# Kernel tuning notes

Measured on AMD Instinct MI355X. Metric: run time of the kernel, lower is better.

## Reference

```python
import jax, jax.numpy as jnp
import numpy as np

# model / batch constants (match init_kwargs and input_specs)
H, D = 32, 128              # num_heads, head_dim
SCALE = 1.0 / float(np.sqrt(D))
BS = 16                     # paged KV-cache block size
NUM_FILL_SEQS, FILL_LEN = 4, 512
NF = NUM_FILL_SEQS * FILL_LEN          # 2048 total fill tokens
G = 16                                  # decode (Generate) sequences
BLOCKS_PER_SEQ = 64
CTX = BLOCKS_PER_SEQ * BS               # 1024 context tokens per decode seq
NB = 1280                               # total cache blocks
T = NF + G                              # 2064 total new tokens this iteration


def setup_inputs() -> dict:
    key = jax.random.key(0)
    kq, kk, kv, kkc, kvc = jax.random.split(key, 5)
    q = jax.random.normal(kq, (T, H, D), jnp.float32)
    k = jax.random.normal(kk, (T, H, D), jnp.float32)
    v = jax.random.normal(kv, (T, H, D), jnp.float32)
    k_cache = jax.random.normal(kkc, (NB, BS, H, D), jnp.float32)
    v_cache = jax.random.normal(kvc, (NB, BS, H, D), jnp.float32)
    # Fill tokens occupy contiguous slots 0..NF-1 (blocks 0..NF/BS-1)
    fill_slots = np.arange(NF, dtype=np.int64)
    # Decode seq g owns blocks [NF/BS + g*BLOCKS_PER_SEQ, ... + BLOCKS_PER_SEQ)
    first_gen_block = NF // BS
    bt = (first_gen_block
          + np.arange(G)[:, None] * BLOCKS_PER_SEQ
          + np.arange(BLOCKS_PER_SEQ)[None, :])            # [G, BLOCKS_PER_SEQ]
    # each decode's new token goes in the last slot of its context
    last = CTX - 1
    gen_slots = bt[:, last // BS] * BS + (last % BS)
    slot_mapping = jnp.asarray(
        np.concatenate([fill_slots, gen_slots]).astype(np.int32))
    block_tables = jnp.asarray(bt.astype(np.int32))
    context_lens = jnp.asarray(np.full((G,), CTX, dtype=np.int32))
    return dict(q=q, k=k, v=v, k_cache=k_cache, v_cache=v_cache,
                slot_mapping=slot_mapping, block_tables=block_tables,
                context_lens=context_lens)


def reference(q, k, v, k_cache, v_cache, slot_mapping, block_tables, context_lens):
    nb, bs = k_cache.shape[0], k_cache.shape[1]
    # vllm_reshape_and_cache: scatter new K/V into the blocked cache by slot id
    kc = k_cache.reshape(nb * bs, H, D).at[slot_mapping].set(k)
    vc = v_cache.reshape(nb * bs, H, D).at[slot_mapping].set(v)
    kcb = kc.reshape(nb, bs, H, D)
    vcb = vc.reshape(nb, bs, H, D)

    # ---- Fill: block-diagonal causal attention (q_len == kv_len fast path) ----
    qf = q[:NF].reshape(NUM_FILL_SEQS, FILL_LEN, H, D)
    kf = k[:NF].reshape(NUM_FILL_SEQS, FILL_LEN, H, D)
    vf = v[:NF].reshape(NUM_FILL_SEQS, FILL_LEN, H, D)
    s = jnp.einsum('bqhd,bkhd->bhqk', qf, kf) * SCALE
    causal = jnp.tril(jnp.ones((FILL_LEN, FILL_LEN), dtype=bool))
    s = jnp.where(causal, s, jnp.finfo(s.dtype).min)
    p = jax.nn.softmax(s, axis=-1)
    fill_out = jnp.einsum('bhqk,bkhd->bqhd', p, vf).reshape(NF, H, D)

    # ---- Generate: vLLM paged attention (1 query token per seq) ----
    qg = q[NF:]                                        # [G, H, D]
    keys = kcb[block_tables].reshape(G, -1, H, D)      # [G, CTX, H, D]
    vals = vcb[block_tables].reshape(G, -1, H, D)
    sg = jnp.einsum('ghd,gshd->ghs', qg, keys) * SCALE
    valid = jnp.arange(keys.shape[1], dtype=jnp.int32)[None, :] < context_lens[:, None]
    sg = jnp.where(valid[:, None, :], sg, jnp.finfo(sg.dtype).min)
    pg = jax.nn.softmax(sg, axis=-1)
    gen_out = jnp.einsum('ghs,gshd->ghd', pg, vals)    # [G, H, D]

    out = jnp.concatenate([fill_out, gen_out], axis=0)
    return out.reshape(T, H * D)
```

## Files before the change

### kernel.cpp

```cpp
#include <hip/hip_runtime.h>
#include <hip/hip_bf16.h>

#define HH 32
#define DD 128
#define HD (HH*DD)
#define NFILL 2048
#define FLEN 512
#define SCALE_F 0.08838834764831845f
#define NEGINF (-1e30f)
#define PSTRIDE 136

typedef short bf16x8 __attribute__((ext_vector_type(8)));
typedef float f32x4 __attribute__((ext_vector_type(4)));

__device__ __forceinline__ short f2bf(float x) {
    union { float f; unsigned u; } c; c.f = x;
    unsigned u = c.u;
    u += 0x7FFFu + ((u >> 16) & 1u);
    return (short)(u >> 16);
}

__device__ __forceinline__ bf16x8 load8_bf16(const float* __restrict__ p) {
    float4 a = *(const float4*)p;
    float4 b = *(const float4*)(p + 4);
    bf16x8 r;
    r[0]=f2bf(a.x); r[1]=f2bf(a.y); r[2]=f2bf(a.z); r[3]=f2bf(a.w);
    r[4]=f2bf(b.x); r[5]=f2bf(b.y); r[6]=f2bf(b.z); r[7]=f2bf(b.w);
    return r;
}

__global__ __launch_bounds__(256)
void gen_kernel(const float* __restrict__ q, const float* __restrict__ k,
                const float* __restrict__ v, const float* __restrict__ kc,
                const float* __restrict__ vc, const int* __restrict__ btab,
                const int* __restrict__ ctxlens, float* __restrict__ ws)
{
    __shared__ int sblk[64];
    __shared__ float accs[16][DD];
    __shared__ float marr[16], larr[16];

    const int bid  = blockIdx.x;
    const int g    = bid >> 6;
    const int h    = (bid >> 1) & 31;
    const int half = bid & 1;
    const int wv   = threadIdx.x >> 6;
    const int lane = threadIdx.x & 63;
    const int g16  = lane >> 4;
    const int li   = lane & 15;
    const int ctx  = ctxlens[g];

    if (threadIdx.x < 64) sblk[threadIdx.x] = btab[g * 64 + threadIdx.x];
    __syncthreads();

    const long qoff = (long)(NFILL + g) * HD + h * DD;
    float qr[8];
    {
        float4 a  = *(const float4*)(q + qoff + li * 8);
        float4 b2 = *(const float4*)(q + qoff + li * 8 + 4);
        qr[0]=a.x; qr[1]=a.y; qr[2]=a.z; qr[3]=a.w;
        qr[4]=b2.x; qr[5]=b2.y; qr[6]=b2.z; qr[7]=b2.w;
    }

    float m = NEGINF, l = 0.f;
    float o[8];
    #pragma unroll
    for (int j = 0; j < 8; ++j) o[j] = 0.f;

    const int wbase = half * 512 + wv * 128;

    #pragma unroll 1
    for (int c = 0; c < 8; ++c) {
        const int pb = wbase + c * 16 + g16 * 4;
        f32x4 ka[4][2], va[4][2];
        #pragma unroll
        for (int i = 0; i < 4; ++i) {
            const int p = pb + i;
            const float* kb; const float* vb;
            if (p == ctx - 1) {
                kb = k + qoff; vb = v + qoff;
            } else {
                const int slot = sblk[p >> 4] * 16 + (p & 15);
                kb = kc + (long)slot * HD + h * DD;
                vb = vc + (long)slot * HD + h * DD;
            }
            ka[i][0] = __builtin_nontemporal_load((const f32x4*)(kb + li * 8));
            ka[i][1] = __builtin_nontemporal_load((const f32x4*)(kb + li * 8 + 4));
            va[i][0] = __builtin_nontemporal_load((const f32x4*)(vb + li * 8));
            va[i][1] = __builtin_nontemporal_load((const f32x4*)(vb + li * 8 + 4));
        }
        float s[4];
        #pragma unroll
        for (int i = 0; i < 4; ++i) {
            float d0 = ka[i][0][0]*qr[0] + ka[i][0][1]*qr[1] + ka[i][0][2]*qr[2] + ka[i][0][3]*qr[3]
                     + ka[i][1][0]*qr[4] + ka[i][1][1]*qr[5] + ka[i][1][2]*qr[6] + ka[i][1][3]*qr[7];
            d0 += __shfl_xor(d0, 1);
            d0 += __shfl_xor(d0, 2);
            d0 += __shfl_xor(d0, 4);
            d0 += __shfl_xor(d0, 8);
            s[i] = d0 * SCALE_F;
        }
        const float mn = fmaxf(m, fmaxf(fmaxf(s[0], s[1]), fmaxf(s[2], s[3])));
        const float sc = __expf(m - mn);
        const float p0 = __expf(s[0] - mn);
        const float p1 = __expf(s[1] - mn);
        const float p2 = __expf(s[2] - mn);
        const float p3 = __expf(s[3] - mn);
        l = l * sc + (p0 + p1 + p2 + p3);
        #pragma unroll
        for (int j = 0; j < 4; ++j) {
            o[j] = o[j]*sc + p0*va[0][0][j] + p1*va[1][0][j]
                           + p2*va[2][0][j] + p3*va[3][0][j];
            o[j+4] = o[j+4]*sc + p0*va[0][1][j] + p1*va[1][1][j]
                               + p2*va[2][1][j] + p3*va[3][1][j];
        }
        m = mn;
    }

    const int pid = wv * 4 + g16;
    #pragma unroll
    for (int j = 0; j < 8; ++j) accs[pid][li * 8 + j] = o[j];
    if (li == 0) { marr[pid] = m; larr[pid] = l; }
    __syncthreads();

    if (threadIdx.x < DD) {
        const int d = threadIdx.x;
        float M = NEGINF;
        #pragma unroll
        for (int t = 0; t < 16; ++t) M = fmaxf(M, marr[t]);
        float L = 0.f, a = 0.f;
        #pragma unroll
        for (int t = 0; t < 16; ++t) {
            const float cc = __expf(marr[t] - M);
            L += cc * larr[t];
            a += cc * accs[t][d];
        }
        const long base = (long)(((g * 32 + h) * 2) + half) * PSTRIDE;
        ws[base + 8 + d] = a;
        if (d == 0) { ws[base] = M; ws[base + 1] = L; }
    }
}

__global__ __launch_bounds__(256)
void merge_kernel(const float* __restrict__ ws, float* __restrict__ out)
{
    const int idx = blockIdx.x * 256 + threadIdx.x;
    const int gh  = idx >> 7;
    const int d   = idx & 127;
    const int g   = gh >> 5;
    const int h   = gh & 31;
    const long b0 = (long)gh * 2 * PSTRIDE;
    const long b1 = b0 + PSTRIDE;
    const float m0 = ws[b0], l0 = ws[b0 + 1];
    const float m1 = ws[b1], l1 = ws[b1 + 1];
    const float M  = fmaxf(m0, m1);
    const float e0 = __expf(m0 - M), e1 = __expf(m1 - M);
    const float num = e0 * ws[b0 + 8 + d] + e1 * ws[b1 + 8 + d];
    const float den = e0 * l0 + e1 * l1;
    out[(long)(NFILL + g) * 4096 + h * DD + d] = num / den;
}

struct QS {
    bf16x8 qf[4];
    float  mrow[4], lsum[4];
    f32x4  o[8];
};

__device__ __forceinline__ void qs_init(QS& S, const float* qbase, int g16) {
    #pragma unroll
    for (int c = 0; c < 4; ++c) S.qf[c] = load8_bf16(qbase + c * 32 + g16 * 8);
    #pragma unroll
    for (int r = 0; r < 4; ++r) { S.mrow[r] = NEGINF; S.lsum[r] = 0.f; }
    #pragma unroll
    for (int n = 0; n < 8; ++n) { S.o[n][0]=0.f; S.o[n][1]=0.f; S.o[n][2]=0.f; S.o[n][3]=0.f; }
}

__device__ __forceinline__ void qs_tile(QS& S, int qt, int k0, int sub,
                                        const char* Kl, const char* Vt2,
                                        char* pbase, int g16, int li) {
    f32x4 sA; sA[0]=0.f; sA[1]=0.f; sA[2]=0.f; sA[3]=0.f;
    f32x4 sB; sB[0]=0.f; sB[1]=0.f; sB[2]=0.f; sB[3]=0.f;
    const int r0 = sub * 32;
    #pragma unroll
    for (int c = 0; c < 4; ++c) {
        const int rA = r0 + li, rB = r0 + li + 16;
        bf16x8 kfA = *(const bf16x8*)(Kl + ((rA * 256 + c * 64 + g16 * 16) ^ ((rA & 7) << 4)));
        bf16x8 kfB = *(const bf16x8*)(Kl + ((rB * 256 + c * 64 + g16 * 16) ^ ((rB & 7) << 4)));
        sA = __builtin_amdgcn_mfma_f32_16x16x32_bf16(S.qf[c], kfA, sA, 0, 0, 0);
        sB = __builtin_amdgcn_mfma_f32_16x16x32_bf16(S.qf[c], kfB, sB, 0, 0, 0);
    }
    float pA[4], pB[4], corr[4];
    #pragma unroll
    for (int r = 0; r < 4; ++r) {
        const int qrow = qt * 16 + g16 * 4 + r;
        float a  = (k0 + li      <= qrow) ? sA[r] * SCALE_F : NEGINF;
        float bb = (k0 + 16 + li <= qrow) ? sB[r] * SCALE_F : NEGINF;
        float rm = fmaxf(a, bb);
        #pragma unroll
        for (int off = 1; off < 16; off <<= 1) rm = fmaxf(rm, __shfl_xor(rm, off));
        const float mn = fmaxf(S.mrow[r], rm);
        corr[r] = __expf(S.mrow[r] - mn);
        pA[r] = __expf(a  - mn);
        pB[r] = __expf(bb - mn);
        float rs = pA[r] + pB[r];
        #pragma unroll
        for (int off = 1; off < 16; off <<= 1) rs += __shfl_xor(rs, off);
        S.lsum[r] = S.lsum[r] * corr[r] + rs;
        S.mrow[r] = mn;
    }
    #pragma unroll
    for (int n = 0; n < 8; ++n)
        #pragma unroll
        for (int r = 0; r < 4; ++r) S.o[n][r] *= corr[r];

    #pragma unroll
    for (int r = 0; r < 4; ++r) {
        const int row = g16 * 4 + r;
        const int xo  = (row & 3) << 4;
        *(short*)(pbase + ((row * 64 + li * 2     ) ^ xo)) = f2bf(pA[r]);
        *(short*)(pbase + ((row * 64 + 32 + li * 2) ^ xo)) = f2bf(pB[r]);
    }
    asm volatile("s_waitcnt lgkmcnt(0)" ::: "memory");
    __builtin_amdgcn_sched_barrier(0);
    bf16x8 pa = *(const bf16x8*)(pbase + ((li * 64 + g16 * 16) ^ ((li & 3) << 4)));

    const int obase = (sub * 4 + g16) * 256 + li * 16;
    #pragma unroll
    for (int n = 0; n < 8; ++n) {
        bf16x8 vf = *(const bf16x8*)(Vt2 + (n * 2048 + obase));
        S.o[n] = __builtin_amdgcn_mfma_f32_16x16x32_bf16(pa, vf, S.o[n], 0, 0, 0);
    }
}

__device__ __forceinline__ void qs_out(QS& S, int qt, int b, int h, int g16, int li,
                                       float* __restrict__ out) {
    float inv[4];
    #pragma unroll
    for (int r = 0; r < 4; ++r) inv[r] = 1.f / S.lsum[r];
    #pragma unroll
    for (int n = 0; n < 8; ++n) {
        #pragma unroll
        for (int r = 0; r < 4; ++r) {
            const int t = b * FLEN + qt * 16 + g16 * 4 + r;
            out[(long)t * 4096 + h * DD + n * 16 + li] = S.o[n][r] * inv[r];
        }
    }
}

__global__ void __launch_bounds__(512, 2)
fill_kernel(const float* __restrict__ q, const float* __restrict__ k,
            const float* __restrict__ v, float* __restrict__ out)
{
    __shared__ short Kl[64 * 128];
    __shared__ short Vt2[8 * 8 * 16 * 8];
    __shared__ short plds[8][16][32];

    const int bid = blockIdx.x;
    const int b   = bid >> 6;
    const int h   = (bid >> 1) & 31;
    const int jh  = bid & 1;
    const int tid  = threadIdx.x;
    const int wv   = tid >> 6;
    const int lane = tid & 63;
    const int g16  = lane >> 4;
    const int li   = lane & 15;

    const int qtA = 2 * wv + jh;
    const int qtB = 31 - qtA;
    const int npA = qtA / 2 + 1;
    const int npB = qtB / 2 + 1;

    QS SA, SB2;
    qs_init(SA,  q + ((long)(b * FLEN + qtA * 16 + li) * HH + h) * DD, g16);
    qs_init(SB2, q + ((long)(b * FLEN + qtB * 16 + li) * HH + h) * DD, g16);

    const int spos = tid >> 4;
    const int sd8  = tid & 15;
    const int vd   = tid & 127;
    const int voct = tid >> 7;

    char* pbase = (char*)&plds[wv][0][0];

    for (int kp = 0; kp < 8; ++kp) {
        const int k0 = kp * 64;
        #pragma unroll
        for (int rr = 0; rr < 2; ++rr) {
            const int row = spos + rr * 32;
            const float* src = k + ((long)(b * FLEN + k0 + row) * HH + h) * DD + sd8 * 8;
            bf16x8 w = load8_bf16(src);
            const int base = row * 256 + sd8 * 16;
            *(bf16x8*)((char*)Kl + (base ^ ((row & 7) << 4))) = w;
        }
        #pragma unroll
        for (int oo = 0; oo < 2; ++oo) {
            const int oct = voct + oo * 4;
            const float* src = v + ((long)(b * FLEN + k0 + oct * 8) * HH + h) * DD + vd;
            bf16x8 w;
            #pragma unroll
            for (int jj = 0; jj < 8; ++jj)
                w[jj] = f2bf(src[(long)jj * HD]);
            *(bf16x8*)((char*)Vt2 + ((vd >> 4) * 2048 + oct * 256 + (vd & 15) * 16)) = w;
        }
        __syncthreads();

        const int kt0 = 2 * kp, kt1 = 2 * kp + 1;
        if (kt0 < npA) qs_tile(SA,  qtA, kt0 * 32, 0, (const char*)Kl, (const char*)Vt2, pbase, g16, li);
        if (kt1 < npA) qs_tile(SA,  qtA, kt1 * 32, 1, (const char*)Kl, (const char*)Vt2, pbase, g16, li);
        if (kt0 < npB) qs_tile(SB2, qtB, kt0 * 32, 0, (const char*)Kl, (const char*)Vt2, pbase, g16, li);
        if (kt1 < npB) qs_tile(SB2, qtB, kt1 * 32, 1, (const char*)Kl, (const char*)Vt2, pbase, g16, li);

        __syncthreads();
    }

    qs_out(SA,  qtA, b, h, g16, li, out);
    qs_out(SB2, qtB, b, h, g16, li, out);
}

extern "C" void kernel_launch(void* const* d_in, const int* in_sizes, int n_in,
                              void* d_out, int out_size, void* d_ws, size_t ws_size,
                              hipStream_t stream) {
    const float* q  = (const float*)d_in[0];
    const float* k  = (const float*)d_in[1];
    const float* v  = (const float*)d_in[2];
    const float* kc = (const float*)d_in[3];
    const float* vc = (const float*)d_in[4];
    const int* btab    = (const int*)d_in[6];
    const int* ctxlens = (const int*)d_in[7];
    float* outp = (float*)d_out;
    float* ws   = (float*)d_ws;

    gen_kernel  <<<dim3(1024), dim3(256), 0, stream>>>(q, k, v, kc, vc, btab, ctxlens, ws);
    merge_kernel<<<dim3(256),  dim3(256), 0, stream>>>(ws, outp);
    fill_kernel <<<dim3(256),  dim3(512), 0, stream>>>(q, k, v, outp);
}
```

Before: 153.0 us.

## Fold merge into fill kernel and register-prefetch next K/V tile

Removes the separate merge kernel launch by having the first 256 threads of each fill block combine the two split-softmax partials for the decode outputs. The fill kernel's K/V staging is split into a global load into registers and a later conversion and LDS write, so the next tile's loads are issued before the current tile's compute (software double buffering). Launch bounds change from 2 to 1 blocks per SM to leave room for the extra prefetch registers, at the cost of possibly lower occupancy.

New measurement: 149.8 us. 2.1% less time.

```diff
diff --git a/kernel.cpp b/kernel.cpp
--- a/kernel.cpp
+++ b/kernel.cpp
@@ -140,25 +140,6 @@
     }
 }
 
-__global__ __launch_bounds__(256)
-void merge_kernel(const float* __restrict__ ws, float* __restrict__ out)
-{
-    const int idx = blockIdx.x * 256 + threadIdx.x;
-    const int gh  = idx >> 7;
-    const int d   = idx & 127;
-    const int g   = gh >> 5;
-    const int h   = gh & 31;
-    const long b0 = (long)gh * 2 * PSTRIDE;
-    const long b1 = b0 + PSTRIDE;
-    const float m0 = ws[b0], l0 = ws[b0 + 1];
-    const float m1 = ws[b1], l1 = ws[b1 + 1];
-    const float M  = fmaxf(m0, m1);
-    const float e0 = __expf(m0 - M), e1 = __expf(m1 - M);
-    const float num = e0 * ws[b0 + 8 + d] + e1 * ws[b1 + 8 + d];
-    const float den = e0 * l0 + e1 * l1;
-    out[(long)(NFILL + g) * 4096 + h * DD + d] = num / den;
-}
-
 struct QS {
     bf16x8 qf[4];
     float  mrow[4], lsum[4];
@@ -246,9 +227,10 @@
     }
 }
 
-__global__ void __launch_bounds__(512, 2)
+__global__ void __launch_bounds__(512, 1)
 fill_kernel(const float* __restrict__ q, const float* __restrict__ k,
-            const float* __restrict__ v, float* __restrict__ out)
+            const float* __restrict__ v, const float* __restrict__ ws,
+            float* __restrict__ out)
 {
     __shared__ short Kl[64 * 128];
     __shared__ short Vt2[8 * 8 * 16 * 8];
@@ -264,6 +246,23 @@
     const int g16  = lane >> 4;
     const int li   = lane & 15;
 
+    if (tid < 256) {
+        const int idx = bid * 256 + tid;
+        const int gh  = idx >> 7;
+        const int d   = idx & 127;
+        const int g   = gh >> 5;
+        const int h2  = gh & 31;
+        const long b0 = (long)gh * 2 * PSTRIDE;
+        const long b1 = b0 + PSTRIDE;
+        const float m0 = ws[b0], l0 = ws[b0 + 1];
+        const float m1 = ws[b1], l1 = ws[b1 + 1];
+        const float M  = fmaxf(m0, m1);
+        const float e0 = __expf(m0 - M), e1 = __expf(m1 - M);
+        const float num = e0 * ws[b0 + 8 + d] + e1 * ws[b1 + 8 + d];
+        const float den = e0 * l0 + e1 * l1;
+        out[(long)(NFILL + g) * 4096 + h2 * DD + d] = num / den;
+    }
+
     const int qtA = 2 * wv + jh;
     const int qtB = 31 - qtA;
     const int npA = qtA / 2 + 1;
@@ -280,27 +279,41 @@
 
     char* pbase = (char*)&plds[wv][0][0];
 
+    float4 kr00, kr01, kr10, kr11;
+    float  vr0[8], vr1[8];
+
+    #define STAGE_LOAD(KP) do { \
+        const float* s0 = k + ((long)(b * FLEN + (KP) * 64 + spos) * HH + h) * DD + sd8 * 8; \
+        kr00 = *(const float4*)s0;  kr01 = *(const float4*)(s0 + 4); \
+        const float* s1 = s0 + (long)32 * HD; \
+        kr10 = *(const float4*)s1;  kr11 = *(const float4*)(s1 + 4); \
+        const float* t0 = v + ((long)(b * FLEN + (KP) * 64 + voct * 8) * HH + h) * DD + vd; \
+        const float* t1 = t0 + (long)32 * HD; \
+        _Pragma("unroll") \
+        for (int jj = 0; jj < 8; ++jj) { vr0[jj] = t0[(long)jj * HD]; vr1[jj] = t1[(long)jj * HD]; } \
+    } while (0)
+
+    #define STAGE_WRITE() do { \
+        bf16x8 w0, w1; \
+        w0[0]=f2bf(kr00.x); w0[1]=f2bf(kr00.y); w0[2]=f2bf(kr00.z); w0[3]=f2bf(kr00.w); \
+        w0[4]=f2bf(kr01.x); w0[5]=f2bf(kr01.y); w0[6]=f2bf(kr01.z); w0[7]=f2bf(kr01.w); \
+        w1[0]=f2bf(kr10.x); w1[1]=f2bf(kr10.y); w1[2]=f2bf(kr10.z); w1[3]=f2bf(kr10.w); \
+        w1[4]=f2bf(kr11.x); w1[5]=f2bf(kr11.y); w1[6]=f2bf(kr11.z); w1[7]=f2bf(kr11.w); \
+        const int row0 = spos, row1 = spos + 32; \
+        *(bf16x8*)((char*)Kl + ((row0 * 256 + sd8 * 16) ^ ((row0 & 7) << 4))) = w0; \
+        *(bf16x8*)((char*)Kl + ((row1 * 256 + sd8 * 16) ^ ((row1 & 7) << 4))) = w1; \
+        bf16x8 u0, u1; \
+        _Pragma("unroll") \
+        for (int jj = 0; jj < 8; ++jj) { u0[jj] = f2bf(vr0[jj]); u1[jj] = f2bf(vr1[jj]); } \
+        *(bf16x8*)((char*)Vt2 + ((vd >> 4) * 2048 + (voct    ) * 256 + (vd & 15) * 16)) = u0; \
+        *(bf16x8*)((char*)Vt2 + ((vd >> 4) * 2048 + (voct + 4) * 256 + (vd & 15) * 16)) = u1; \
+    } while (0)
+
+    STAGE_LOAD(0);
     for (int kp = 0; kp < 8; ++kp) {
-        const int k0 = kp * 64;
-        #pragma unroll
-        for (int rr = 0; rr < 2; ++rr) {
-            const int row = spos + rr * 32;
-            const float* src = k + ((long)(b * FLEN + k0 + row) * HH + h) * DD + sd8 * 8;
-            bf16x8 w = load8_bf16(src);
-            const int base = row * 256 + sd8 * 16;
-            *(bf16x8*)((char*)Kl + (base ^ ((row & 7) << 4))) = w;
-        }
-        #pragma unroll
-        for (int oo = 0; oo < 2; ++oo) {
-            const int oct = voct + oo * 4;
-            const float* src = v + ((long)(b * FLEN + k0 + oct * 8) * HH + h) * DD + vd;
-            bf16x8 w;
-            #pragma unroll
-            for (int jj = 0; jj < 8; ++jj)
-                w[jj] = f2bf(src[(long)jj * HD]);
-            *(bf16x8*)((char*)Vt2 + ((vd >> 4) * 2048 + oct * 256 + (vd & 15) * 16)) = w;
-        }
+        STAGE_WRITE();
         __syncthreads();
+        if (kp < 7) STAGE_LOAD(kp + 1);
 
         const int kt0 = 2 * kp, kt1 = 2 * kp + 1;
         if (kt0 < npA) qs_tile(SA,  qtA, kt0 * 32, 0, (const char*)Kl, (const char*)Vt2, pbase, g16, li);
@@ -328,7 +341,6 @@
     float* outp = (float*)d_out;
     float* ws   = (float*)d_ws;
 
-    gen_kernel  <<<dim3(1024), dim3(256), 0, stream>>>(q, k, v, kc, vc, btab, ctxlens, ws);
-    merge_kernel<<<dim3(256),  dim3(256), 0, stream>>>(ws, outp);
-    fill_kernel <<<dim3(256),  dim3(512), 0, stream>>>(q, k, v, outp);
-}
+    gen_kernel <<<dim3(1024), dim3(256), 0, stream>>>(q, k, v, kc, vc, btab, ctxlens, ws);
+    fill_kernel<<<dim3(256),  dim3(512), 0, stream>>>(q, k, v, ws, outp);
+}
```
